# Kernel tuning notes

Hardware: AMD Instinct MI355X
Metric: run time of the kernel (lower is better)

## Reference

```python
import jax, jax.numpy as jnp
import numpy as np

EPS = 1e-20
TEMP = 0.07
PATCH = 64
STEP = 32  # patch_size * overlap(0.5)


def zero_softmax(x, eps=1e-5):
    # ZeroSoftmax: ((exp(x)-1)^2) / (sum + eps), maps x==0 -> exactly 0 weight
    e = jnp.square(jnp.exp(x) - 1.0)
    return e / (jnp.sum(e, axis=-1, keepdims=True) + eps)


def _scaling_mask(H, W, p, step):
    # constant overlap-count mask from CRW.compute_scaling_mask (static shapes)
    sm = np.zeros((H, W), np.float32)
    for i in range(0, H - step, step):
        for j in range(0, W - step, step):
            sm[i:i + p, j:j + p] += 1.0
    return jnp.asarray(sm)


def _window_sums(m, p, step):
    # m: (B,T,SP,H,W) -> sliding-window sums (B,T,SP,nH,nW) via integral image
    ii = jnp.cumsum(jnp.cumsum(m, axis=-2), axis=-1)
    ii = jnp.pad(ii, ((0, 0), (0, 0), (0, 0), (1, 0), (1, 0)))
    H = m.shape[-2]
    nH = (H - p) // step + 1
    lo = jnp.arange(nH) * step
    hi = lo + p
    r_hi = ii[..., hi, :]   # (B,T,SP,nH,W+1)
    r_lo = ii[..., lo, :]
    return r_hi[..., hi] - r_hi[..., lo] - r_lo[..., hi] + r_lo[..., lo]


def setup_inputs() -> dict:
    key = jax.random.key(0)
    k1, k2, k3 = jax.random.split(key, 3)
    B, T, H, W = 2, 4, 256, 256
    nH = (H - PATCH) // STEP + 1  # 7
    N = nH * nH                   # 49 patches
    Cenc, D, SP = 512, 128, 64
    feats = jax.random.normal(k1, (B, N, Cenc, T), jnp.float32)
    W_head = jax.random.normal(k2, (Cenc, D), jnp.float32) / np.sqrt(Cenc)
    sp_mask = jax.random.randint(k3, (B, T, H, W), 0, SP, jnp.int32)
    return {"feats": feats, "W_head": W_head, "sp_mask": sp_mask, "max_sp_num": SP}


def reference(feats, W_head, sp_mask, max_sp_num):
    B, N, Cenc, T = feats.shape
    H, W = sp_mask.shape[-2:]
    SP = max_sp_num

    # --- pixels_to_nodes tail: projection head + L2 normalize over channel dim ---
    q = jnp.einsum('bnct,cd->bndt', feats, W_head)            # (B,N,128,T)
    nrm = jnp.maximum(jnp.linalg.norm(q, axis=2, keepdims=True), 1e-12)
    q = q / nrm
    q = jnp.transpose(q, (0, 2, 3, 1))                        # (B,128,T,N)

    # --- patches_to_sp_embeddings: windowed superpixel pooling ---
    oh = (sp_mask[:, :, None, :, :] ==
          jnp.arange(SP, dtype=sp_mask.dtype)[None, None, :, None, None]
          ).astype(jnp.float32)                               # (B,T,SP,H,W)
    sm = _scaling_mask(H, W, PATCH, STEP)                     # (H,W)
    ws = _window_sums(oh / sm, PATCH, STEP)                   # (B,T,SP,nH,nW)
    denom = jnp.sum(oh, axis=(-1, -2)) + EPS                  # (B,T,SP)
    wts = jnp.transpose(ws, (0, 1, 3, 4, 2)) / denom[:, :, None, None, :]
    wts = wts.reshape(B, T, N, SP)                            # (B,T,N,SP)
    q_sp = jnp.einsum('bdtn,btns->bdts', q, wts)              # (B,128,T,SP)

    # --- affinity + zero_softmax stochastic matrices ---
    As = jnp.einsum('bdtn,bdtm->btnm', q_sp[:, :, :-1], q_sp[:, :, 1:])  # (B,T-1,SP,SP)
    A12 = zero_softmax(As / TEMP)
    A21 = zero_softmax(jnp.swapaxes(As, -1, -2) / TEMP)

    # --- palindrome random walks + cross-entropy to cycle-consistency targets ---
    tgt = jnp.tile(jnp.arange(SP), B)
    loss = jnp.float32(0.0)
    AAs = []
    for i in range(1, T - 1):
        mats = [A12[:, k] for k in range(i + 1)] + [A21[:, k] for k in range(i, -1, -1)]
        aa = mats[0]
        for m in mats[1:]:
            aa = aa @ m
        AAs.append(aa)
        logits = jnp.log(aa + EPS).reshape(B * SP, SP)
        logp = jax.nn.log_softmax(logits, axis=-1)
        loss = loss + jnp.mean(-logp[jnp.arange(B * SP), tgt])
    return loss, jnp.stack(AAs)
```

## Files before the change

kernel.cpp:

```cpp
#include <hip/hip_runtime.h>
#include <hip/hip_bf16.h>

constexpr int NWIN = 49;
constexpr int QLD  = 52;

constexpr int OFF_WS   = 0;
constexpr int OFF_Q    = 26624;
constexpr int OFF_QSP  = 79872;
constexpr int OFF_A12  = 145408;
constexpr int OFF_A12T = 169984;
constexpr int OFF_A21  = 194560;
constexpr int OFF_A21T = 219136;
constexpr int OFF_R1T  = 251904;
constexpr int OFF_L    = 260096;
constexpr int OFF_BAR  = 276480;

__global__ void __launch_bounds__(256, 1)
k_front(const int* __restrict__ mask, const float* __restrict__ feats,
        const float* __restrict__ Wh, float* __restrict__ ws, float* __restrict__ q) {
    if (blockIdx.x < 392) {
        int win = blockIdx.x % NWIN;
        int bt  = blockIdx.x / NWIN;
        int wy = win / 7, wx = win % 7;
        __shared__ float loc[64];
        if (threadIdx.x < 64) loc[threadIdx.x] = 0.f;
        __syncthreads();
        const int* base = mask + bt * 65536 + (wy * 32) * 256 + wx * 32;
        #pragma unroll
        for (int it = 0; it < 16; ++it) {
            int idx = it * 256 + (int)threadIdx.x;
            int r = idx >> 6, c = idx & 63;
            int s = base[r * 256 + c];
            int y = wy * 32 + r, x = wx * 32 + c;
            float w = 1.f;
            if (y >= 32 && y < 224) w *= 0.5f;
            if (x >= 32 && x < 224) w *= 0.5f;
            atomicAdd(&loc[s], w);
        }
        __syncthreads();
        if (threadIdx.x < 64) {
            ws[(bt * 64 + (int)threadIdx.x) * QLD + win] = loc[threadIdx.x];
        } else if (win == 0) {
            int s = threadIdx.x & 63;
            int col = 49 + (int)(threadIdx.x >> 6) - 1;
            ws[(bt * 64 + s) * QLD + col] = 0.f;
        }
    } else {
        int bid = blockIdx.x - 392;
        int n = bid % NWIN, b = bid / NWIN;
        __shared__ float4 f4[512];
        __shared__ float4 psum4[256];
        __shared__ float4 red4[2];
        const float4* fp4 = (const float4*)(feats + (size_t)(b * NWIN + n) * 2048);
        for (int i = threadIdx.x; i < 512; i += 256) f4[i] = fp4[i];
        __syncthreads();

        int d = threadIdx.x & 127, ch = threadIdx.x >> 7;
        float a0 = 0.f, a1 = 0.f, a2 = 0.f, a3 = 0.f;
        const float* wp = Wh + d;
        int c0 = ch * 256;
        #pragma unroll 8
        for (int c = c0; c < c0 + 256; ++c) {
            float w = wp[c * 128];
            float4 fv = f4[c];
            a0 += fv.x * w; a1 += fv.y * w; a2 += fv.z * w; a3 += fv.w * w;
        }
        psum4[threadIdx.x] = make_float4(a0, a1, a2, a3);
        __syncthreads();

        float4 A;
        if (threadIdx.x < 128) {
            float4 p0 = psum4[threadIdx.x], p1 = psum4[128 + threadIdx.x];
            A = make_float4(p0.x + p1.x, p0.y + p1.y, p0.z + p1.z, p0.w + p1.w);
            float sx = A.x * A.x, sy = A.y * A.y, sz = A.z * A.z, sw = A.w * A.w;
            for (int off = 32; off; off >>= 1) {
                sx += __shfl_down(sx, off); sy += __shfl_down(sy, off);
                sz += __shfl_down(sz, off); sw += __shfl_down(sw, off);
            }
            if ((threadIdx.x & 63) == 0) red4[threadIdx.x >> 6] = make_float4(sx, sy, sz, sw);
        }
        __syncthreads();
        if (threadIdx.x < 128) {
            float4 r0 = red4[0], r1 = red4[1];
            float ix = 1.f / fmaxf(sqrtf(r0.x + r1.x), 1e-12f);
            float iy = 1.f / fmaxf(sqrtf(r0.y + r1.y), 1e-12f);
            float iz = 1.f / fmaxf(sqrtf(r0.z + r1.z), 1e-12f);
            float iw = 1.f / fmaxf(sqrtf(r0.w + r1.w), 1e-12f);
            float* qb = q + (size_t)(b * 128 + d) * 4 * QLD + n;
            qb[0 * QLD] = A.x * ix;
            qb[1 * QLD] = A.y * iy;
            qb[2 * QLD] = A.z * iz;
            qb[3 * QLD] = A.w * iw;
        }
    }
}

__global__ void k_qsp(const float* __restrict__ q, const float* __restrict__ wsg,
                      float* __restrict__ qsp, float* __restrict__ out,
                      int* __restrict__ bar) {
    if (blockIdx.x == 0 && threadIdx.x < 4) {
        bar[threadIdx.x] = 0;
        if (threadIdx.x == 0) out[0] = 0.f;
    }
    int tid = blockIdx.x * 256 + threadIdx.x;
    int s = tid & 63;
    int d = (tid >> 6) & 127;
    int t = (tid >> 13) & 3;
    int b = tid >> 15;
    const float4* qrow = (const float4*)(q + (size_t)((b * 128 + d) * 4 + t) * QLD);
    const float4* wrow = (const float4*)(wsg + (size_t)((b * 4 + t) * 64 + s) * QLD);
    float acc = 0.f, den = 0.f;
    #pragma unroll
    for (int i = 0; i < 13; ++i) {
        float4 w = wrow[i];
        float4 qv = qrow[i];
        den += w.x + w.y + w.z + w.w;
        acc += qv.x * w.x + qv.y * w.y + qv.z * w.z + qv.w * w.w;
    }
    qsp[tid] = acc / (den + 1e-20f);
}


__device__ __forceinline__ void dump_mat(float* M, const float4* v) {
    #pragma unroll
    for (int it = 0; it < 4; ++it) {
        int idx = it * 256 + (int)threadIdx.x;
        int r = idx >> 4, c4 = (idx & 15) << 2;
        *(float4*)&M[r * 64 + (c4 ^ ((r & 15) << 2))] = v[it];
    }
}

__device__ __forceinline__ void stage1(float* M, const float* __restrict__ G) {
    const float4* g = (const float4*)G;
    float4 v[4];
    #pragma unroll
    for (int it = 0; it < 4; ++it) v[it] = g[it * 256 + (int)threadIdx.x];
    dump_mat(M, v);
}

__device__ __forceinline__ void stage2(float* Ma, float* Mb,
                                       const float* __restrict__ Ga,
                                       const float* __restrict__ Gb) {
    const float4* ga = (const float4*)Ga;
    const float4* gb = (const float4*)Gb;
    float4 va[4], vb[4];
    #pragma unroll
    for (int it = 0; it < 4; ++it) {
        int idx = it * 256 + (int)threadIdx.x;
        va[it] = ga[idx];
        vb[it] = gb[idx];
    }
    dump_mat(Ma, va);
    dump_mat(Mb, vb);
}

__device__ __forceinline__ void mm256_sw(float* acc, const float* Ra, const float* Rb) {
    int tid = threadIdx.x;
    int nl = tid >> 4, ml = tid & 15;
    int sxa = nl << 2, sxb = ml << 2;
    #pragma unroll
    for (int i = 0; i < 16; ++i) acc[i] = 0.f;
    #pragma unroll 4
    for (int k0 = 0; k0 < 64; k0 += 4) {
        float4 av[4], bv[4];
        #pragma unroll
        for (int i = 0; i < 4; ++i)
            av[i] = *(const float4*)&Ra[(nl + 16 * i) * 64 + (k0 ^ sxa)];
        #pragma unroll
        for (int j = 0; j < 4; ++j)
            bv[j] = *(const float4*)&Rb[(ml + 16 * j) * 64 + (k0 ^ sxb)];
        #pragma unroll
        for (int i = 0; i < 4; ++i)
            #pragma unroll
            for (int j = 0; j < 4; ++j)
                acc[i * 4 + j] += av[i].x * bv[j].x + av[i].y * bv[j].y
                                + av[i].z * bv[j].z + av[i].w * bv[j].w;
    }
}

__device__ __forceinline__ void wr256_sw(float* M, const float* acc) {
    int nl = threadIdx.x >> 4, ml = threadIdx.x & 15;
    #pragma unroll
    for (int i = 0; i < 4; ++i)
        #pragma unroll
        for (int j = 0; j < 4; ++j) {
            int r = nl + 16 * i, k = ml + 16 * j;
            M[r * 64 + (((k & ~3) ^ ((r & 15) << 2)) | (k & 3))] = acc[i * 4 + j];
        }
}

__device__ __forceinline__ void store_mat(float* __restrict__ G, const float* acc) {
    int nl = threadIdx.x >> 4, ml = threadIdx.x & 15;
    #pragma unroll
    for (int i = 0; i < 4; ++i)
        #pragma unroll
        for (int j = 0; j < 4; ++j)
            G[(nl + 16 * i) * 64 + ml + 16 * j] = acc[i * 4 + j];
}

__device__ __forceinline__ void store_loss(const float* acc, float* __restrict__ aa,
                                           float* __restrict__ out, float* red) {
    int tid = threadIdx.x;
    int nl = tid >> 4, ml = tid & 15;
    #pragma unroll
    for (int i = 0; i < 4; ++i)
        #pragma unroll
        for (int j = 0; j < 4; ++j)
            aa[(nl + 16 * i) * 64 + (ml + 16 * j)] = acc[i * 4 + j];
    int l = tid & 63;
    float part = 0.f;
    #pragma unroll
    for (int i = 0; i < 4; ++i) {
        float rsum = acc[i * 4 + 0] + acc[i * 4 + 1] + acc[i * 4 + 2] + acc[i * 4 + 3];
        rsum += __shfl_down(rsum, 8, 16);
        rsum += __shfl_down(rsum, 4, 16);
        rsum += __shfl_down(rsum, 2, 16);
        rsum += __shfl_down(rsum, 1, 16);
        float dv = __shfl(acc[5 * i], (l & 48) | nl, 64);
        if ((l & 15) == 0) part += logf(rsum + 6.4e-19f) - logf(dv + 1e-20f);
    }
    for (int off = 32; off; off >>= 1) part += __shfl_down(part, off);
    if (l == 0) red[tid >> 6] = part;
    __syncthreads();
    if (tid == 0) atomicAdd(out, (red[0] + red[1] + red[2] + red[3]) * (1.f / 128.f));
}

__device__ __forceinline__ void gbar(int* cnt, int target) {
    __threadfence();
    __syncthreads();
    if (threadIdx.x == 0) {
        __hip_atomic_fetch_add(cnt, 1, __ATOMIC_ACQ_REL, __HIP_MEMORY_SCOPE_AGENT);
        while (__hip_atomic_load(cnt, __ATOMIC_ACQUIRE, __HIP_MEMORY_SCOPE_AGENT) < target)
            __builtin_amdgcn_s_sleep(2);
    }
    __syncthreads();
    __threadfence();
}

__global__ void __launch_bounds__(256, 1)
k_tail(const float* __restrict__ qsp,
       float* __restrict__ a12, float* __restrict__ a12T,
       float* __restrict__ a21, float* __restrict__ a21T,
       float* __restrict__ wsR1T, float* __restrict__ wsL,
       float* __restrict__ out, int* __restrict__ bar) {
    __shared__ float SM[16384];
    float* M0 = SM;
    float* M1 = SM + 4096;
    float* M2 = SM + 8192;
    float* M3 = SM + 12288;
    const int tid = threadIdx.x;
    const int blk = blockIdx.x;

    {
        int t = blk % 3, b = blk / 3;
        float4* qaT4 = (float4*)SM;
        float4* qbT4 = (float4*)SM + 2048;
        {
            const float4* gA = (const float4*)(qsp + (size_t)(b * 4 + t) * 8192);
            const float4* gB = (const float4*)(qsp + (size_t)(b * 4 + t + 1) * 8192);
            float* qaF = (float*)qaT4;
            float* qbF = (float*)qbT4;
            #pragma unroll
            for (int it = 0; it < 8; ++it) {
                int idx = it * 256 + tid;
                int d = idx >> 4, s0 = (idx & 15) << 2;
                float4 va = gA[idx];
                float4 vb = gB[idx];
                int g = d >> 2, c = d & 3;
                #pragma unroll
                for (int u = 0; u < 4; ++u) {
                    int s = s0 + u;
                    int w = (s * 32 + (g ^ (s & 31))) * 4 + c;
                    float fa = (u == 0) ? va.x : (u == 1) ? va.y : (u == 2) ? va.z : va.w;
                    float fb = (u == 0) ? vb.x : (u == 1) ? vb.y : (u == 2) ? vb.z : vb.w;
                    qaF[w] = fa;
                    qbF[w] = fb;
                }
            }
        }
        __syncthreads();

        const int nl = tid >> 4, ml = tid & 15;
        float acc[16];
        #pragma unroll
        for (int i = 0; i < 16; ++i) acc[i] = 0.f;
        #pragma unroll 8
        for (int k4 = 0; k4 < 32; ++k4) {
            float4 av[4], bv[4];
            #pragma unroll
            for (int i = 0; i < 4; ++i) { int n = nl + 16 * i; av[i] = qaT4[n * 32 + (k4 ^ (n & 31))]; }
            #pragma unroll
            for (int j = 0; j < 4; ++j) { int m = ml + 16 * j; bv[j] = qbT4[m * 32 + (k4 ^ (m & 31))]; }
            #pragma unroll
            for (int i = 0; i < 4; ++i)
                #pragma unroll
                for (int j = 0; j < 4; ++j)
                    acc[i * 4 + j] += av[i].x * bv[j].x + av[i].y * bv[j].y
                                    + av[i].z * bv[j].z + av[i].w * bv[j].w;
        }
        __syncthreads();

        float* eb = (float*)qaT4;
        float* rs = (float*)qbT4;
        float* cs = rs + 64;
        #pragma unroll
        for (int i = 0; i < 4; ++i)
            #pragma unroll
            for (int j = 0; j < 4; ++j) {
                int n = nl + 16 * i, m = ml + 16 * j;
                float x = acc[i * 4 + j] * (1.f / 0.07f);
                float e = expf(x) - 1.f;
                eb[n * 65 + m] = e * e;
            }
        __syncthreads();
        if (tid < 128) {
            int r = tid & 63; bool isrow = tid < 64;
            float a = 0.f;
            #pragma unroll
            for (int k = 0; k < 64; ++k) a += isrow ? eb[r * 65 + k] : eb[k * 65 + r];
            (isrow ? rs : cs)[r] = a + 1e-5f;
        }
        __syncthreads();
        float* p12  = a12  + (b * 3 + t) * 4096;
        float* p12T = a12T + (b * 3 + t) * 4096;
        float* p21  = a21  + (b * 3 + t) * 4096;
        float* p21T = a21T + (b * 3 + t) * 4096;
        #pragma unroll
        for (int i = 0; i < 4; ++i)
            #pragma unroll
            for (int j = 0; j < 4; ++j) {
                int n = nl + 16 * i, m = ml + 16 * j;
                float v   = eb[n * 65 + m];
                float v12 = v / rs[n];
                float v21 = v / cs[m];
                if (t == 0) {
                    p12 [n * 64 + m] = v12;
                    p21T[n * 64 + m] = v21;
                } else {
                    p12T[m * 64 + n] = v12;
                    p21 [m * 64 + n] = v21;
                }
            }
    }
    gbar(bar + 0, 6);
    if (blk >= 4) return;

    int b = blk >> 1, odd = blk & 1;
    if (!odd) {
        stage2(M0, M1, a12 + (b * 3 + 0) * 4096, a12T + (b * 3 + 1) * 4096);
        __syncthreads();
        float acc[16];
        mm256_sw(acc, M0, M1);
        wr256_sw(M2, acc);
        stage1(M3, a12T + (b * 3 + 2) * 4096);
        __syncthreads();
        float acc2[16];
        mm256_sw(acc2, M2, M3);
        store_mat(wsL + b * 4096, acc2);
    } else {
        stage2(M0, M1, a21T + (b * 3 + 0) * 4096, a21 + (b * 3 + 1) * 4096);
        __syncthreads();
        float acc[16];
        mm256_sw(acc, M0, M1);
        store_mat(wsR1T + b * 4096, acc);
        wr256_sw(M2, acc);
        stage1(M3, a21 + (b * 3 + 2) * 4096);
        __syncthreads();
        float acc2[16];
        mm256_sw(acc2, M2, M3);
        wr256_sw(M1, acc2);
    }
    gbar(bar + 1, 4);

    if (!odd) {
        stage1(M3, wsR1T + b * 4096);
        __syncthreads();
        float acc[16];
        mm256_sw(acc, M2, M3);
        store_loss(acc, out + 1 + b * 4096, out, M0);
    } else {
        stage1(M0, wsL + b * 4096);
        __syncthreads();
        float acc[16];
        mm256_sw(acc, M0, M1);
        store_loss(acc, out + 1 + (2 + b) * 4096, out, M2);
    }
}

extern "C" void kernel_launch(void* const* d_in, const int* in_sizes, int n_in,
                              void* d_out, int out_size, void* d_ws, size_t ws_size,
                              hipStream_t stream) {
    const float* feats = (const float*)d_in[0];
    const float* Wh    = (const float*)d_in[1];
    const int*   mask  = (const int*)d_in[2];
    float* out = (float*)d_out;
    float* ws  = (float*)d_ws;

    float* ws_sums = ws + OFF_WS;
    float* q       = ws + OFF_Q;
    float* qsp     = ws + OFF_QSP;
    float* a12     = ws + OFF_A12;
    float* a12T    = ws + OFF_A12T;
    float* a21     = ws + OFF_A21;
    float* a21T    = ws + OFF_A21T;
    float* wsR1T   = ws + OFF_R1T;
    float* wsL     = ws + OFF_L;
    int*   bar     = (int*)(ws + OFF_BAR);

    k_front<<<392 + 2 * NWIN, 256, 0, stream>>>(mask, feats, Wh, ws_sums, q);
    k_qsp<<<256, 256, 0, stream>>>(q, ws_sums, qsp, out, bar);
    k_tail<<<6, 256, 0, stream>>>(qsp, a12, a12T, a21, a21T,
                                  wsR1T, wsL, out, bar);
}
```

Baseline: 110.7 us.

## Store q_sp pre-swizzled and split projection over four channel chunks

The q_sp kernel now writes its output directly in the transposed, XOR-swizzled shared-memory layout that the affinity kernel expects. The affinity kernel can then copy it with plain float4 loads instead of scattering scalars into LDS. Separately, the projection head splits the 512 input channels into four chunks, each thread computing two output dims, with a four-way partial-sum reduction. The aim is to cut LDS scatter cost and improve load balance, at the price of scattered global stores in k_qsp and more shared memory for the partial sums.

```diff
diff --git a/kernel.cpp b/kernel.cpp
--- a/kernel.cpp
+++ b/kernel.cpp
@@ -49,29 +49,38 @@
         int bid = blockIdx.x - 392;
         int n = bid % NWIN, b = bid / NWIN;
         __shared__ float4 f4[512];
-        __shared__ float4 psum4[256];
+        __shared__ float4 psum4[512];
         __shared__ float4 red4[2];
         const float4* fp4 = (const float4*)(feats + (size_t)(b * NWIN + n) * 2048);
         for (int i = threadIdx.x; i < 512; i += 256) f4[i] = fp4[i];
         __syncthreads();
 
-        int d = threadIdx.x & 127, ch = threadIdx.x >> 7;
+        int dl = threadIdx.x & 63, ch = threadIdx.x >> 6;
         float a0 = 0.f, a1 = 0.f, a2 = 0.f, a3 = 0.f;
-        const float* wp = Wh + d;
-        int c0 = ch * 256;
+        float b0 = 0.f, b1 = 0.f, b2 = 0.f, b3 = 0.f;
+        const float* wpa = Wh + dl;
+        const float* wpb = Wh + dl + 64;
+        int c0 = ch * 128;
         #pragma unroll 8
-        for (int c = c0; c < c0 + 256; ++c) {
-            float w = wp[c * 128];
+        for (int c = c0; c < c0 + 128; ++c) {
+            float w0 = wpa[c * 128];
+            float w1 = wpb[c * 128];
             float4 fv = f4[c];
-            a0 += fv.x * w; a1 += fv.y * w; a2 += fv.z * w; a3 += fv.w * w;
-        }
-        psum4[threadIdx.x] = make_float4(a0, a1, a2, a3);
+            a0 += fv.x * w0; a1 += fv.y * w0; a2 += fv.z * w0; a3 += fv.w * w0;
+            b0 += fv.x * w1; b1 += fv.y * w1; b2 += fv.z * w1; b3 += fv.w * w1;
+        }
+        psum4[ch * 128 + dl]      = make_float4(a0, a1, a2, a3);
+        psum4[ch * 128 + dl + 64] = make_float4(b0, b1, b2, b3);
         __syncthreads();
 
         float4 A;
         if (threadIdx.x < 128) {
-            float4 p0 = psum4[threadIdx.x], p1 = psum4[128 + threadIdx.x];
-            A = make_float4(p0.x + p1.x, p0.y + p1.y, p0.z + p1.z, p0.w + p1.w);
+            float4 p0 = psum4[threadIdx.x],       p1 = psum4[128 + threadIdx.x];
+            float4 p2 = psum4[256 + threadIdx.x], p3 = psum4[384 + threadIdx.x];
+            A = make_float4((p0.x + p1.x) + (p2.x + p3.x),
+                            (p0.y + p1.y) + (p2.y + p3.y),
+                            (p0.z + p1.z) + (p2.z + p3.z),
+                            (p0.w + p1.w) + (p2.w + p3.w));
             float sx = A.x * A.x, sy = A.y * A.y, sz = A.z * A.z, sw = A.w * A.w;
             for (int off = 32; off; off >>= 1) {
                 sx += __shfl_down(sx, off); sy += __shfl_down(sy, off);
@@ -86,7 +95,7 @@
             float iy = 1.f / fmaxf(sqrtf(r0.y + r1.y), 1e-12f);
             float iz = 1.f / fmaxf(sqrtf(r0.z + r1.z), 1e-12f);
             float iw = 1.f / fmaxf(sqrtf(r0.w + r1.w), 1e-12f);
-            float* qb = q + (size_t)(b * 128 + d) * 4 * QLD + n;
+            float* qb = q + (size_t)(b * 128 + (int)threadIdx.x) * 4 * QLD + n;
             qb[0 * QLD] = A.x * ix;
             qb[1 * QLD] = A.y * iy;
             qb[2 * QLD] = A.z * iz;
@@ -102,11 +111,11 @@
         bar[threadIdx.x] = 0;
         if (threadIdx.x == 0) out[0] = 0.f;
     }
-    int tid = blockIdx.x * 256 + threadIdx.x;
-    int s = tid & 63;
-    int d = (tid >> 6) & 127;
-    int t = (tid >> 13) & 3;
-    int b = tid >> 15;
+    int gid = blockIdx.x * 256 + threadIdx.x;
+    int d = gid & 127;
+    int s = (gid >> 7) & 63;
+    int t = (gid >> 13) & 3;
+    int b = gid >> 15;
     const float4* qrow = (const float4*)(q + (size_t)((b * 128 + d) * 4 + t) * QLD);
     const float4* wrow = (const float4*)(wsg + (size_t)((b * 4 + t) * 64 + s) * QLD);
     float acc = 0.f, den = 0.f;
@@ -117,7 +126,8 @@
         den += w.x + w.y + w.z + w.w;
         acc += qv.x * w.x + qv.y * w.y + qv.z * w.z + qv.w * w.w;
     }
-    qsp[tid] = acc / (den + 1e-20f);
+    int w = (s * 32 + ((d >> 2) ^ (s & 31))) * 4 + (d & 3);
+    qsp[(size_t)(b * 4 + t) * 8192 + w] = acc / (den + 1e-20f);
 }
 
 
@@ -258,24 +268,11 @@
         {
             const float4* gA = (const float4*)(qsp + (size_t)(b * 4 + t) * 8192);
             const float4* gB = (const float4*)(qsp + (size_t)(b * 4 + t + 1) * 8192);
-            float* qaF = (float*)qaT4;
-            float* qbF = (float*)qbT4;
             #pragma unroll
             for (int it = 0; it < 8; ++it) {
                 int idx = it * 256 + tid;
-                int d = idx >> 4, s0 = (idx & 15) << 2;
-                float4 va = gA[idx];
-                float4 vb = gB[idx];
-                int g = d >> 2, c = d & 3;
-                #pragma unroll
-                for (int u = 0; u < 4; ++u) {
-                    int s = s0 + u;
-                    int w = (s * 32 + (g ^ (s & 31))) * 4 + c;
-                    float fa = (u == 0) ? va.x : (u == 1) ? va.y : (u == 2) ? va.z : va.w;
-                    float fb = (u == 0) ? vb.x : (u == 1) ? vb.y : (u == 2) ? vb.z : vb.w;
-                    qaF[w] = fa;
-                    qbF[w] = fb;
-                }
+                qaT4[idx] = gA[idx];
+                qbT4[idx] = gB[idx];
             }
         }
         __syncthreads();
```

New measurement: 107.3 us. 1.03x faster.
